# Optimization experiments

Measured on AMD Instinct MI355X. Metric: run time of the kernel, lower is better.

Reference implementation:

```python
import jax, jax.numpy as jnp
import numpy as np

OUTPUT_SIZE = 200
IOU_THRESHOLD = 0.5
SCORE_THRESHOLD = 0.01


def setup_inputs() -> dict:
    key = jax.random.key(0)
    k1, k2, k3 = jax.random.split(key, 3)
    B, N, C = 8, 2048, 80
    # well-formed boxes in [0,1]: (min_xy, max_xy)
    centers = jax.random.uniform(k1, (B, N, 2))
    sizes = jax.random.uniform(k2, (B, N, 2), minval=0.02, maxval=0.3)
    boxes = jnp.concatenate([centers - sizes / 2, centers + sizes / 2], axis=-1)
    scores = jax.random.uniform(k3, (B, N, C))
    x = jnp.concatenate([boxes, scores], axis=-1)  # [B, N, 4+C]
    return {"x": x}


def _box_iou(b):
    # b: [N, 4] (x1, y1, x2, y2) -> [N, N] IoU
    lt = jnp.maximum(b[:, None, :2], b[None, :, :2])
    rb = jnp.minimum(b[:, None, 2:], b[None, :, 2:])
    wh = jnp.maximum(rb - lt, 0.0)
    inter = wh[..., 0] * wh[..., 1]
    area = (b[:, 2] - b[:, 0]) * (b[:, 3] - b[:, 1])
    union = area[:, None] + area[None, :] - inter
    return inter / jnp.maximum(union, 1e-8)


def _nms_one_class(iou_b, scores_bc):
    # iou_b: [N, N] (shared across classes), scores_bc: [N]
    N = scores_bc.shape[0]
    order = jnp.argsort(-scores_bc)            # descending score order
    s_sorted = scores_bc[order]
    keep0 = s_sorted > SCORE_THRESHOLD
    pos = jnp.arange(N)

    def body(i, keep):
        row = iou_b[order[i]][order]           # IoU of i-th ranked box vs all, in sorted order
        sup = keep[i]                          # only a kept box suppresses others
        return keep & ~((row > IOU_THRESHOLD) & (pos > i) & sup)

    keep = jax.lax.fori_loop(0, N, body, keep0)
    # cap to max_output_size_per_class: keep only first OUTPUT_SIZE kept boxes
    rank = jnp.cumsum(keep.astype(jnp.int32))
    keep = keep & (rank <= OUTPUT_SIZE)
    sel_scores = jnp.where(keep, s_sorted, -jnp.inf)
    return sel_scores, order


def _combined_nms_one_batch(boxes_b, scores_b, iou_b):
    # boxes_b: [N,4], scores_b: [N,C], iou_b: [N,N]
    N, C = scores_b.shape
    sel_scores, order = jax.vmap(_nms_one_class, in_axes=(None, 1))(iou_b, scores_b)  # [C,N] each
    flat_scores = sel_scores.reshape(C * N)
    top_scores, top_idx = jax.lax.top_k(flat_scores, OUTPUT_SIZE)  # global top across classes
    cls = top_idx // N
    pos = top_idx % N
    box_idx = order[cls, pos]                  # original box indices
    top_boxes = jnp.clip(boxes_b[box_idx], 0.0, 1.0)  # clip_boxes=True
    valid = jnp.isfinite(top_scores)
    out = jnp.concatenate([
        cls.astype(jnp.float32)[:, None],
        top_scores[:, None],
        top_boxes,
    ], axis=-1)                                # [OUTPUT_SIZE, 6] = (cls, score, x1, y1, x2, y2)
    return jnp.where(valid[:, None], out, 0.0)


def reference(x):
    boxes = x[..., :4]                         # [B, N, 4]
    scores = x[..., 4:]                        # [B, N, C]
    iou = jax.vmap(_box_iou)(boxes)            # [B, N, N] (boxes shared across classes)
    return jax.vmap(_combined_nms_one_batch)(boxes, scores, iou)  # [B, OUTPUT_SIZE, 6]
```

## Files before the change

kernel.cpp:

```cpp
#include <hip/hip_runtime.h>
#include <stdint.h>

typedef unsigned long long u64;
typedef unsigned int u32;

#define NB 8
#define NN 2048
#define NC 80
#define ROW 84
#define OUT_K 200
#define IOU_T 0.5f
#define SCORE_T 0.01f
#define TGT 896
#define POOL 1024

__device__ __forceinline__ void ce_desc(u64* a, int i, int j, int k) {
    u64 a0 = a[i], a1 = a[i + j];
    bool up = ((i & k) == 0);
    if (up ? (a0 < a1) : (a0 > a1)) { a[i] = a1; a[i + j] = a0; }
}

__device__ __forceinline__ void ceg(u64& x, u64& y, bool up) {
    u64 a0 = x, a1 = y;
    if (up ? (a0 < a1) : (a0 > a1)) { x = a1; y = a0; }
}

__device__ __forceinline__ void wave_rounds512(u64* a, int base, int k, int jhi, int lane) {
    for (int j = jhi; j > 0; j >>= 1) {
        #pragma unroll
        for (int p = 0; p < 4; p++) {
            int r = lane + p * 64;
            int low = r & (j - 1);
            int high = (r & ~(j - 1)) << 1;
            ce_desc(a, base + (high | low), j, k);
        }
        __builtin_amdgcn_wave_barrier();
    }
}

__device__ __forceinline__ void wave_rounds256(u64* a, int base, int k, int jhi, int lane) {
    for (int j = jhi; j > 0; j >>= 1) {
        #pragma unroll
        for (int p = 0; p < 2; p++) {
            int r = lane + p * 64;
            int low = r & (j - 1);
            int high = (r & ~(j - 1)) << 1;
            ce_desc(a, base + (high | low), j, k);
        }
        __builtin_amdgcn_wave_barrier();
    }
}

__device__ __forceinline__ void pair_merge256(u64* a, int base, int off, int lane) {
    #pragma unroll
    for (int p0 = 0; p0 < 4; p0++) {
        int p = lane + p0 * 64;
        u64 xv = a[base + p];
        u64 yv = a[base + off + 255 - p];
        a[base + p] = xv > yv ? xv : yv;
    }
    __builtin_amdgcn_wave_barrier();
    wave_rounds256(a, base, 0x40000000, 128, lane);
}

__device__ __forceinline__ void sort2048(u64* key, int tid, int lane, int wv) {
    const int base = wv * 512;
    for (int k = 2; k <= 512; k <<= 1)
        wave_rounds512(key, base, k, k >> 1, lane);
    __syncthreads();
    #pragma unroll
    for (int p = 0; p < 4; p++) {
        int r = tid + p * 256;
        int low = r & 511, high = (r & ~511) << 1;
        ce_desc(key, high | low, 512, 1024);
    }
    __syncthreads();
    wave_rounds512(key, base, 1024, 256, lane);
    __syncthreads();
    #pragma unroll
    for (int p = 0; p < 4; p++) {
        int r = tid + p * 256;
        int low = r & 1023, high = (r & ~1023) << 1;
        ce_desc(key, high | low, 1024, 2048);
    }
    __syncthreads();
    #pragma unroll
    for (int p = 0; p < 4; p++) {
        int r = tid + p * 256;
        int low = r & 511, high = (r & ~511) << 1;
        ce_desc(key, high | low, 512, 2048);
    }
    __syncthreads();
    wave_rounds512(key, base, 2048, 256, lane);
    __syncthreads();
}

__device__ __forceinline__ void sort1024(u64* a, int tid, int lane, int wv) {
    const int t4 = tid * 4;
    const int sb = wv * 256;
    {
        u64 v0 = a[t4], v1 = a[t4 + 1], v2 = a[t4 + 2], v3 = a[t4 + 3];
        ceg(v0, v1, true);
        ceg(v2, v3, false);
        const bool d4 = ((t4 & 4) == 0);
        ceg(v0, v2, d4); ceg(v1, v3, d4);
        ceg(v0, v1, d4); ceg(v2, v3, d4);
        a[t4] = v0; a[t4 + 1] = v1; a[t4 + 2] = v2; a[t4 + 3] = v3;
    }
    __builtin_amdgcn_wave_barrier();
    for (int k = 8; k <= 256; k <<= 1) {
        for (int j = k >> 1; j >= 4; j >>= 1) {
            #pragma unroll
            for (int p = 0; p < 2; p++) {
                int r = lane + p * 64;
                int low = r & (j - 1);
                int high = (r & ~(j - 1)) << 1;
                ce_desc(a, sb + (high | low), j, k);
            }
            __builtin_amdgcn_wave_barrier();
        }
        {
            u64 v0 = a[t4], v1 = a[t4 + 1], v2 = a[t4 + 2], v3 = a[t4 + 3];
            const bool d = ((t4 & k) == 0);
            ceg(v0, v2, d); ceg(v1, v3, d);
            ceg(v0, v1, d); ceg(v2, v3, d);
            a[t4] = v0; a[t4 + 1] = v1; a[t4 + 2] = v2; a[t4 + 3] = v3;
        }
        __builtin_amdgcn_wave_barrier();
    }
    __syncthreads();
    #pragma unroll
    for (int p = 0; p < 2; p++) {
        int r = tid + p * 256;
        int low = r & 255, high = (r & ~255) << 1;
        ce_desc(a, high | low, 256, 512);
    }
    __syncthreads();
    for (int j = 128; j >= 4; j >>= 1) {
        #pragma unroll
        for (int p = 0; p < 2; p++) {
            int r = lane + p * 64;
            int low = r & (j - 1);
            int high = (r & ~(j - 1)) << 1;
            ce_desc(a, sb + (high | low), j, 512);
        }
        __builtin_amdgcn_wave_barrier();
    }
    {
        u64 v0 = a[t4], v1 = a[t4 + 1], v2 = a[t4 + 2], v3 = a[t4 + 3];
        const bool d = ((t4 & 512) == 0);
        ceg(v0, v2, d); ceg(v1, v3, d);
        ceg(v0, v1, d); ceg(v2, v3, d);
        a[t4] = v0; a[t4 + 1] = v1; a[t4 + 2] = v2; a[t4 + 3] = v3;
    }
    __syncthreads();
    #pragma unroll
    for (int p = 0; p < 2; p++) {
        int r = tid + p * 256;
        int low = r & 511, high = (r & ~511) << 1;
        ce_desc(a, high | low, 512, 1024);
    }
    __syncthreads();
    #pragma unroll
    for (int p = 0; p < 2; p++) {
        int r = tid + p * 256;
        int low = r & 255, high = (r & ~255) << 1;
        ce_desc(a, high | low, 256, 1024);
    }
    __syncthreads();
    for (int j = 128; j >= 4; j >>= 1) {
        #pragma unroll
        for (int p = 0; p < 2; p++) {
            int r = lane + p * 64;
            int low = r & (j - 1);
            int high = (r & ~(j - 1)) << 1;
            ce_desc(a, sb + (high | low), j, 1024);
        }
        __builtin_amdgcn_wave_barrier();
    }
    {
        u64 v0 = a[t4], v1 = a[t4 + 1], v2 = a[t4 + 2], v3 = a[t4 + 3];
        const bool d = ((t4 & 1024) == 0);
        ceg(v0, v2, d); ceg(v1, v3, d);
        ceg(v0, v1, d); ceg(v2, v3, d);
        a[t4] = v0; a[t4 + 1] = v1; a[t4 + 2] = v2; a[t4 + 3] = v3;
    }
    __syncthreads();
}

__device__ __forceinline__ bool iou_gt_half(float4 a, float aa, float4 b, float ab) {
    float ltx = fmaxf(a.x, b.x);
    float lty = fmaxf(a.y, b.y);
    float rbx = fminf(a.z, b.z);
    float rby = fminf(a.w, b.w);
    float wd = fmaxf(__fsub_rn(rbx, ltx), 0.0f);
    float hd = fmaxf(__fsub_rn(rby, lty), 0.0f);
    float inter = __fmul_rn(wd, hd);
    float uni = __fsub_rn(__fadd_rn(aa, ab), inter);
    float m = fmaxf(uni, 1e-8f);
    float d2 = __fmul_rn(2.0f, inter);
    bool sup = d2 > m;
    if (sup && (__fsub_rn(d2, m) <= __fmul_rn(m, 1.2e-7f)))
        sup = __fdiv_rn(inter, m) > IOU_T;
    return sup;
}

__device__ __forceinline__ void prefetch512(const u64* cand, const float* xb,
        float4* pbox, float* parea, int tid) {
    #pragma unroll
    for (int r = 0; r < 2; r++) {
        int i = r * 256 + tid;
        u64 k = cand[i];
        u32 orig = 2047u - (u32)(k & 0x7FFu);
        float4 bx = *(const float4*)(xb + (size_t)orig * ROW);
        pbox[i] = bx;
        parea[i] = __fmul_rn(__fsub_rn(bx.z, bx.x), __fsub_rn(bx.w, bx.y));
    }
    __syncthreads();
}

__device__ __forceinline__ int greedy(const u64* cand, int maxch, const float* xb,
        const float4* pbox, const float* parea,
        float4* s_cbox, float* s_car,
        float4* kept_box, float* kept_area, u64* kept_key,
        u64* s_sup, int* s_kept, int* s_done, int tid, int lane, int wv,
        int keptc_in) {
    if (tid == 0) { *s_kept = keptc_in; *s_done = 0; }
    __syncthreads();
    int keptc = keptc_in;
    for (int ch = 0; ch < maxch; ch++) {
        int n = ch * 64 + lane;
        u64 mykey = cand[n];
        float sc = __uint_as_float((u32)(mykey >> 32));
        bool valid = sc > SCORE_T;
        u64 vball = __ballot(valid);
        if (vball == 0ULL) break;

        float4 bx; float ar;
        const float4* cb; const float* ca;
        if (ch < 8) {
            bx = pbox[n];
            ar = parea[n];
            cb = pbox + ch * 64;
            ca = parea + ch * 64;
        } else {
            u32 orig = 2047u - (u32)(mykey & 0x7FFu);
            bx = *(const float4*)(xb + (size_t)orig * ROW);
            ar = __fmul_rn(__fsub_rn(bx.z, bx.x), __fsub_rn(bx.w, bx.y));
            if (wv == 0) { s_cbox[lane] = bx; s_car[lane] = ar; }
            __builtin_amdgcn_wave_barrier();
            cb = s_cbox; ca = s_car;
        }

        u64 colmask = 0ULL;
        if (wv == 0) {
            #pragma unroll 4
            for (int j = 0; j < 64; j++) {
                bool s = iou_gt_half(bx, ar, cb[j], ca[j]);
                colmask |= ((u64)s) << j;
            }
        } else {
            bool supA = false;
            int t = wv - 1;
            for (; t + 9 < keptc; t += 12) {
                float4 kb0 = kept_box[t],     kb1 = kept_box[t + 3];
                float4 kb2 = kept_box[t + 6], kb3 = kept_box[t + 9];
                float ka0 = kept_area[t],     ka1 = kept_area[t + 3];
                float ka2 = kept_area[t + 6], ka3 = kept_area[t + 9];
                bool s0 = iou_gt_half(bx, ar, kb0, ka0);
                bool s1 = iou_gt_half(bx, ar, kb1, ka1);
                bool s2 = iou_gt_half(bx, ar, kb2, ka2);
                bool s3 = iou_gt_half(bx, ar, kb3, ka3);
                supA = supA | ((s0 | s1) | (s2 | s3));
            }
            for (; t < keptc; t += 3)
                supA = supA | iou_gt_half(bx, ar, kept_box[t], kept_area[t]);
            u64 supm = __ballot(supA);
            if (lane == 0) s_sup[wv] = supm;
        }
        __syncthreads();

        if (wv == 0) {
            u64 alive = vball & ~s_sup[1] & ~s_sup[2] & ~s_sup[3];
            int kept = keptc;
            u64 keptbits = 0ULL;
            int donef = 0;
            while (alive) {
                int bsel = (int)__builtin_ctzll(alive);
                keptbits |= 1ULL << bsel;
                kept++;
                if (kept >= OUT_K) { donef = 1; break; }
                alive &= alive - 1;
                if (!alive) break;
                alive &= ~__ballot(((colmask >> bsel) & 1ULL) != 0ULL);
            }
            u32 rank = (u32)__popcll(keptbits & ((1ULL << lane) - 1ULL));
            if ((keptbits >> lane) & 1ULL) {
                int idx = keptc + (int)rank;
                kept_key[idx] = mykey;
                kept_box[idx] = bx;
                kept_area[idx] = ar;
            }
            if (lane == 0) { *s_kept = kept; if (donef) *s_done = 1; }
        }
        __syncthreads();
        keptc = *s_kept;
        if (*s_done) break;
        if (__popcll(vball) < 64) break;
    }
    __syncthreads();
    return keptc;
}

__global__ __launch_bounds__(256) void transpose_kernel(
        const float* __restrict__ x, float* __restrict__ st) {
    const int t = blockIdx.x;
    const int b = t >> 5;
    const int rb = t & 31;
    const int tid = threadIdx.x;
    __shared__ float lds[64 * 85];

    const float* src = x + ((size_t)b * NN + (size_t)rb * 64) * ROW;
    #pragma unroll
    for (int q = 0; q < 6; q++) {
        int i4 = q * 256 + tid;
        if (i4 < 1344) {
            float4 v = *(const float4*)(src + (size_t)i4 * 4);
            int r = i4 / 21;
            int kq = (i4 % 21) * 4;
            float* d = lds + r * 85 + kq;
            d[0] = v.x; d[1] = v.y; d[2] = v.z; d[3] = v.w;
        }
    }
    __syncthreads();
    const int n0 = rb * 64;
    #pragma unroll
    for (int q = 0; q < 20; q++) {
        int j = q * 256 + tid;
        int c = j >> 6;
        int r = j & 63;
        st[(size_t)(b * NC + c) * NN + n0 + r] = lds[r * 85 + 4 + c];
    }
}

__global__ __launch_bounds__(256) void nms_kernel(
        const float* __restrict__ x, const float* __restrict__ scores_t,
        u64* __restrict__ cand_key) {
    const int bc = blockIdx.x;
    const int b = bc / NC;
    const int c = bc % NC;
    const int tid = threadIdx.x;
    const int lane = tid & 63;
    const int wv = tid >> 6;

    __shared__ __align__(16) u64 arr[2048];
    u64* comp = arr;
    u32* hist = (u32*)(arr + 1024);
    __shared__ __align__(16) float4 s_pbox[512];
    __shared__ float s_parea[512];
    __shared__ __align__(16) float4 s_cbox[64];
    __shared__ float s_car[64];
    __shared__ float4 kept_box[OUT_K];
    __shared__ float kept_area[OUT_K];
    __shared__ u64 kept_key[OUT_K];
    __shared__ u64 s_sup[4];
    __shared__ u32 s_wsum[4];
    __shared__ u32 s_cnt, s_m;
    __shared__ int s_kept, s_done, s_thr;

    const float* xb = x + (size_t)b * NN * ROW;
    const float* sct = scores_t + (size_t)(b * NC + c) * NN;

    hist[tid] = 0;
    __syncthreads();
    float scv[8];
    #pragma unroll
    for (int w = 0; w < 8; w++) {
        int n = w * 256 + tid;
        float sc = sct[n];
        scv[w] = sc;
        int bin = (int)(sc * 256.0f); bin = bin > 255 ? 255 : bin;
        atomicAdd(&hist[bin], 1u);
    }
    __syncthreads();

    u32 cnt_mine = hist[tid];
    u32 incl = cnt_mine;
    #pragma unroll
    for (int off = 1; off < 64; off <<= 1) {
        u32 v = __shfl_down(incl, off, 64);
        if (lane + off < 64) incl += v;
    }
    if (lane == 0) s_wsum[wv] = incl;
    __syncthreads();
    u32 above = 0;
    #pragma unroll
    for (int w = 0; w < 4; w++) above += (w > wv) ? s_wsum[w] : 0;
    const u32 suf = incl + above;

    if (tid == 0) s_thr = 2;
    __syncthreads();
    if (suf >= TGT && suf - cnt_mine < TGT) s_thr = tid;
    __syncthreads();
    int t1 = s_thr;
    if (tid == t1) s_m = suf;
    __syncthreads();
    u32 m_tot = s_m;

    bool fb = (m_tot > POOL);
    int kept = 0;
    if (!fb) {
        if (tid == 0) s_cnt = 0;
        __syncthreads();
        #pragma unroll
        for (int w = 0; w < 8; w++) {
            float sc = scv[w];
            int bin = (int)(sc * 256.0f); bin = bin > 255 ? 255 : bin;
            if (bin >= t1) {
                int n = w * 256 + tid;
                u32 p = atomicAdd(&s_cnt, 1u);
                comp[p] = ((u64)__float_as_uint(sc) << 32) | (u64)(2047 - n);
            }
        }
        __syncthreads();
        for (int i = tid; i < POOL; i += 256) if (i >= (int)m_tot) comp[i] = 0ULL;
        __syncthreads();
        sort1024(comp, tid, lane, wv);
        prefetch512(comp, xb, s_pbox, s_parea, tid);
        kept = greedy(comp, POOL / 64, xb, s_pbox, s_parea, s_cbox, s_car,
                      kept_box, kept_area, kept_key,
                      s_sup, &s_kept, &s_done, tid, lane, wv, 0);

        while (kept < OUT_K && t1 > 2) {
            u32 T2 = m_tot + TGT;
            if (tid == 0) s_thr = 2;
            __syncthreads();
            if (suf >= T2 && suf - cnt_mine < T2) s_thr = tid;
            __syncthreads();
            int t2 = s_thr;
            if (tid == t2) s_m = suf;
            __syncthreads();
            u32 m2 = s_m;
            u32 size = m2 - m_tot;
            if (size == 0) break;
            if (size > POOL) { fb = true; break; }
            if (tid == 0) s_cnt = 0;
            __syncthreads();
            #pragma unroll
            for (int w = 0; w < 8; w++) {
                float sc = scv[w];
                int bin = (int)(sc * 256.0f); bin = bin > 255 ? 255 : bin;
                if (bin >= t2 && bin < t1) {
                    int n = w * 256 + tid;
                    u32 p = atomicAdd(&s_cnt, 1u);
                    comp[p] = ((u64)__float_as_uint(sc) << 32) | (u64)(2047 - n);
                }
            }
            __syncthreads();
            for (int i = tid; i < POOL; i += 256) if (i >= (int)size) comp[i] = 0ULL;
            __syncthreads();
            sort1024(comp, tid, lane, wv);
            prefetch512(comp, xb, s_pbox, s_parea, tid);
            kept = greedy(comp, POOL / 64, xb, s_pbox, s_parea, s_cbox, s_car,
                          kept_box, kept_area, kept_key,
                          s_sup, &s_kept, &s_done, tid, lane, wv, kept);
            m_tot = m2; t1 = t2;
        }
    }
    if (fb) {
        __syncthreads();
        #pragma unroll
        for (int w = 0; w < 8; w++) {
            int n = w * 256 + tid;
            arr[n] = ((u64)__float_as_uint(scv[w]) << 32) | (u64)(2047 - n);
        }
        __syncthreads();
        sort2048(arr, tid, lane, wv);
        prefetch512(arr, xb, s_pbox, s_parea, tid);
        kept = greedy(arr, 32, xb, s_pbox, s_parea, s_cbox, s_car,
                      kept_box, kept_area, kept_key,
                      s_sup, &s_kept, &s_done, tid, lane, wv, 0);
    }

    const int base_o = bc * OUT_K;
    if (tid < OUT_K) {
        u64 ok = 0ULL;
        if (tid < kept) {
            u64 kk = kept_key[tid];
            u32 flat = (u32)(c * OUT_K + tid);
            u32 orig = 2047u - (u32)(kk & 0x7FFu);
            ok = (kk & 0xFFFFFFFF00000000ULL) |
                 ((u64)(0x3FFFu - flat) << 11) | (u64)orig;
        }
        cand_key[base_o + tid] = ok;
    }
}

__global__ __launch_bounds__(256) void merge8_kernel(u64* __restrict__ cand_key) {
    const int blk = blockIdx.x;
    const int b = blk / 10;
    const int g = blk % 10;
    const int tid = threadIdx.x;
    const int lane = tid & 63;
    const int wv = tid >> 6;
    __shared__ __align__(16) u64 seg[2048];

    u64* src = cand_key + (size_t)(b * NC + g * 8) * OUT_K;

    #pragma unroll
    for (int q = 0; q < 8; q++) {
        seg[q * 256 + tid] = (tid < OUT_K) ? src[q * OUT_K + tid] : 0ULL;
    }
    __syncthreads();
    pair_merge256(seg, wv * 512, 256, lane);
    __syncthreads();
    if (wv < 2) pair_merge256(seg, wv * 1024, 512, lane);
    __syncthreads();
    if (wv == 0) pair_merge256(seg, 0, 1024, lane);
    __syncthreads();
    src[tid] = seg[tid];
}

__global__ __launch_bounds__(256) void final_kernel(
        const float* __restrict__ x, const u64* __restrict__ cand_key,
        float* __restrict__ out) {
    const int b = blockIdx.x;
    const int tid = threadIdx.x;
    const int lane = tid & 63;
    const int wv = tid >> 6;
    __shared__ __align__(16) u64 seg[2560];

    #pragma unroll
    for (int q = 0; q < 10; q++) {
        seg[q * 256 + tid] = cand_key[(size_t)(b * NC + q * 8) * OUT_K + tid];
    }
    __syncthreads();
    pair_merge256(seg, wv * 512, 256, lane);
    __syncthreads();
    if (wv == 0) pair_merge256(seg, 0, 512, lane);
    else if (wv == 1) pair_merge256(seg, 1024, 512, lane);
    else if (wv == 2) pair_merge256(seg, 2048, 256, lane);
    __syncthreads();
    if (wv == 0) pair_merge256(seg, 0, 1024, lane);
    __syncthreads();
    if (wv == 0) pair_merge256(seg, 0, 2048, lane);
    __syncthreads();

    const float* xb = x + (size_t)b * NN * ROW;
    if (tid < OUT_K) {
        u64 kk = seg[tid];
        float* o = out + ((size_t)b * OUT_K + tid) * 6;
        if (kk == 0ULL) {
            o[0] = 0.f; o[1] = 0.f; o[2] = 0.f; o[3] = 0.f; o[4] = 0.f; o[5] = 0.f;
        } else {
            u32 lo = (u32)(kk & 0xFFFFFFFFu);
            u32 flat = 0x3FFFu - ((lo >> 11) & 0x3FFFu);
            int cls = flat / OUT_K;
            u32 n = lo & 0x7FFu;
            float scf = __uint_as_float((u32)(kk >> 32));
            float4 bx = *(const float4*)(xb + (size_t)n * ROW);
            o[0] = (float)cls;
            o[1] = scf;
            o[2] = fminf(fmaxf(bx.x, 0.0f), 1.0f);
            o[3] = fminf(fmaxf(bx.y, 0.0f), 1.0f);
            o[4] = fminf(fmaxf(bx.z, 0.0f), 1.0f);
            o[5] = fminf(fmaxf(bx.w, 0.0f), 1.0f);
        }
    }
}

extern "C" void kernel_launch(void* const* d_in, const int* in_sizes, int n_in,
                              void* d_out, int out_size, void* d_ws, size_t ws_size,
                              hipStream_t stream) {
    const float* x = (const float*)d_in[0];
    float* out = (float*)d_out;
    u64* cand_key = (u64*)d_ws;
    float* scores_t = (float*)((char*)d_ws + 1024 * 1024);
    transpose_kernel<<<NB * 32, 256, 0, stream>>>(x, scores_t);
    nms_kernel<<<NB * NC, 256, 0, stream>>>(x, scores_t, cand_key);
    merge8_kernel<<<NB * 10, 256, 0, stream>>>(cand_key);
    final_kernel<<<NB, 256, 0, stream>>>(x, cand_key, out);
}
```

Before: 143.8 us.

## Double NMS block to 512 threads, split greedy work across eight waves

The per-class NMS kernel moves from 256 to 512 threads. The greedy column-mask IoU work is split between waves 0 and 4, and checks against already kept boxes are spread over six waves instead of three. Candidate compaction now uses wave-aggregated ballot plus a single atomic per wave instead of one atomic per element. The sorts keep their 4-wave structure, with the upper waves idle except in the cross-wave compare stages, which adds occupancy and barrier costs for the extra threads.

```diff
diff --git a/kernel.cpp b/kernel.cpp
--- a/kernel.cpp
+++ b/kernel.cpp
@@ -64,126 +64,135 @@
 }
 
 __device__ __forceinline__ void sort2048(u64* key, int tid, int lane, int wv) {
-    const int base = wv * 512;
-    for (int k = 2; k <= 512; k <<= 1)
-        wave_rounds512(key, base, k, k >> 1, lane);
-    __syncthreads();
-    #pragma unroll
-    for (int p = 0; p < 4; p++) {
-        int r = tid + p * 256;
+    if (wv < 4) {
+        const int base = wv * 512;
+        for (int k = 2; k <= 512; k <<= 1)
+            wave_rounds512(key, base, k, k >> 1, lane);
+    }
+    __syncthreads();
+    #pragma unroll
+    for (int p = 0; p < 2; p++) {
+        int r = tid + p * 512;
         int low = r & 511, high = (r & ~511) << 1;
         ce_desc(key, high | low, 512, 1024);
     }
     __syncthreads();
-    wave_rounds512(key, base, 1024, 256, lane);
-    __syncthreads();
-    #pragma unroll
-    for (int p = 0; p < 4; p++) {
-        int r = tid + p * 256;
+    if (wv < 4) wave_rounds512(key, wv * 512, 1024, 256, lane);
+    __syncthreads();
+    #pragma unroll
+    for (int p = 0; p < 2; p++) {
+        int r = tid + p * 512;
         int low = r & 1023, high = (r & ~1023) << 1;
         ce_desc(key, high | low, 1024, 2048);
     }
     __syncthreads();
     #pragma unroll
-    for (int p = 0; p < 4; p++) {
-        int r = tid + p * 256;
+    for (int p = 0; p < 2; p++) {
+        int r = tid + p * 512;
         int low = r & 511, high = (r & ~511) << 1;
         ce_desc(key, high | low, 512, 2048);
     }
     __syncthreads();
-    wave_rounds512(key, base, 2048, 256, lane);
+    if (wv < 4) wave_rounds512(key, wv * 512, 2048, 256, lane);
     __syncthreads();
 }
 
 __device__ __forceinline__ void sort1024(u64* a, int tid, int lane, int wv) {
-    const int t4 = tid * 4;
-    const int sb = wv * 256;
+    if (wv < 4) {
+        const int t4 = tid * 4;
+        const int sb = wv * 256;
+        {
+            u64 v0 = a[t4], v1 = a[t4 + 1], v2 = a[t4 + 2], v3 = a[t4 + 3];
+            ceg(v0, v1, true);
+            ceg(v2, v3, false);
+            const bool d4 = ((t4 & 4) == 0);
+            ceg(v0, v2, d4); ceg(v1, v3, d4);
+            ceg(v0, v1, d4); ceg(v2, v3, d4);
+            a[t4] = v0; a[t4 + 1] = v1; a[t4 + 2] = v2; a[t4 + 3] = v3;
+        }
+        __builtin_amdgcn_wave_barrier();
+        for (int k = 8; k <= 256; k <<= 1) {
+            for (int j = k >> 1; j >= 4; j >>= 1) {
+                #pragma unroll
+                for (int p = 0; p < 2; p++) {
+                    int r = lane + p * 64;
+                    int low = r & (j - 1);
+                    int high = (r & ~(j - 1)) << 1;
+                    ce_desc(a, sb + (high | low), j, k);
+                }
+                __builtin_amdgcn_wave_barrier();
+            }
+            {
+                u64 v0 = a[t4], v1 = a[t4 + 1], v2 = a[t4 + 2], v3 = a[t4 + 3];
+                const bool d = ((t4 & k) == 0);
+                ceg(v0, v2, d); ceg(v1, v3, d);
+                ceg(v0, v1, d); ceg(v2, v3, d);
+                a[t4] = v0; a[t4 + 1] = v1; a[t4 + 2] = v2; a[t4 + 3] = v3;
+            }
+            __builtin_amdgcn_wave_barrier();
+        }
+    }
+    __syncthreads();
     {
-        u64 v0 = a[t4], v1 = a[t4 + 1], v2 = a[t4 + 2], v3 = a[t4 + 3];
-        ceg(v0, v1, true);
-        ceg(v2, v3, false);
-        const bool d4 = ((t4 & 4) == 0);
-        ceg(v0, v2, d4); ceg(v1, v3, d4);
-        ceg(v0, v1, d4); ceg(v2, v3, d4);
-        a[t4] = v0; a[t4 + 1] = v1; a[t4 + 2] = v2; a[t4 + 3] = v3;
-    }
-    __builtin_amdgcn_wave_barrier();
-    for (int k = 8; k <= 256; k <<= 1) {
-        for (int j = k >> 1; j >= 4; j >>= 1) {
+        int r = tid;
+        int low = r & 255, high = (r & ~255) << 1;
+        ce_desc(a, high | low, 256, 512);
+    }
+    __syncthreads();
+    if (wv < 4) {
+        const int t4 = tid * 4;
+        const int sb = wv * 256;
+        for (int j = 128; j >= 4; j >>= 1) {
             #pragma unroll
             for (int p = 0; p < 2; p++) {
                 int r = lane + p * 64;
                 int low = r & (j - 1);
                 int high = (r & ~(j - 1)) << 1;
-                ce_desc(a, sb + (high | low), j, k);
+                ce_desc(a, sb + (high | low), j, 512);
             }
             __builtin_amdgcn_wave_barrier();
         }
         {
             u64 v0 = a[t4], v1 = a[t4 + 1], v2 = a[t4 + 2], v3 = a[t4 + 3];
-            const bool d = ((t4 & k) == 0);
+            const bool d = ((t4 & 512) == 0);
             ceg(v0, v2, d); ceg(v1, v3, d);
             ceg(v0, v1, d); ceg(v2, v3, d);
             a[t4] = v0; a[t4 + 1] = v1; a[t4 + 2] = v2; a[t4 + 3] = v3;
         }
-        __builtin_amdgcn_wave_barrier();
-    }
-    __syncthreads();
-    #pragma unroll
-    for (int p = 0; p < 2; p++) {
-        int r = tid + p * 256;
-        int low = r & 255, high = (r & ~255) << 1;
-        ce_desc(a, high | low, 256, 512);
-    }
-    __syncthreads();
-    for (int j = 128; j >= 4; j >>= 1) {
-        #pragma unroll
-        for (int p = 0; p < 2; p++) {
-            int r = lane + p * 64;
-            int low = r & (j - 1);
-            int high = (r & ~(j - 1)) << 1;
-            ce_desc(a, sb + (high | low), j, 512);
-        }
-        __builtin_amdgcn_wave_barrier();
-    }
+    }
+    __syncthreads();
     {
-        u64 v0 = a[t4], v1 = a[t4 + 1], v2 = a[t4 + 2], v3 = a[t4 + 3];
-        const bool d = ((t4 & 512) == 0);
-        ceg(v0, v2, d); ceg(v1, v3, d);
-        ceg(v0, v1, d); ceg(v2, v3, d);
-        a[t4] = v0; a[t4 + 1] = v1; a[t4 + 2] = v2; a[t4 + 3] = v3;
-    }
-    __syncthreads();
-    #pragma unroll
-    for (int p = 0; p < 2; p++) {
-        int r = tid + p * 256;
+        int r = tid;
         int low = r & 511, high = (r & ~511) << 1;
         ce_desc(a, high | low, 512, 1024);
     }
     __syncthreads();
-    #pragma unroll
-    for (int p = 0; p < 2; p++) {
-        int r = tid + p * 256;
+    {
+        int r = tid;
         int low = r & 255, high = (r & ~255) << 1;
         ce_desc(a, high | low, 256, 1024);
     }
     __syncthreads();
-    for (int j = 128; j >= 4; j >>= 1) {
-        #pragma unroll
-        for (int p = 0; p < 2; p++) {
-            int r = lane + p * 64;
-            int low = r & (j - 1);
-            int high = (r & ~(j - 1)) << 1;
-            ce_desc(a, sb + (high | low), j, 1024);
-        }
-        __builtin_amdgcn_wave_barrier();
-    }
-    {
-        u64 v0 = a[t4], v1 = a[t4 + 1], v2 = a[t4 + 2], v3 = a[t4 + 3];
-        const bool d = ((t4 & 1024) == 0);
-        ceg(v0, v2, d); ceg(v1, v3, d);
-        ceg(v0, v1, d); ceg(v2, v3, d);
-        a[t4] = v0; a[t4 + 1] = v1; a[t4 + 2] = v2; a[t4 + 3] = v3;
+    if (wv < 4) {
+        const int t4 = tid * 4;
+        const int sb = wv * 256;
+        for (int j = 128; j >= 4; j >>= 1) {
+            #pragma unroll
+            for (int p = 0; p < 2; p++) {
+                int r = lane + p * 64;
+                int low = r & (j - 1);
+                int high = (r & ~(j - 1)) << 1;
+                ce_desc(a, sb + (high | low), j, 1024);
+            }
+            __builtin_amdgcn_wave_barrier();
+        }
+        {
+            u64 v0 = a[t4], v1 = a[t4 + 1], v2 = a[t4 + 2], v3 = a[t4 + 3];
+            const bool d = ((t4 & 1024) == 0);
+            ceg(v0, v2, d); ceg(v1, v3, d);
+            ceg(v0, v1, d); ceg(v2, v3, d);
+            a[t4] = v0; a[t4 + 1] = v1; a[t4 + 2] = v2; a[t4 + 3] = v3;
+        }
     }
     __syncthreads();
 }
@@ -205,23 +214,35 @@
     return sup;
 }
 
+__device__ __forceinline__ float bcast(float v, int sl) {
+    return __int_as_float(__builtin_amdgcn_readlane(__float_as_int(v), sl));
+}
+
 __device__ __forceinline__ void prefetch512(const u64* cand, const float* xb,
         float4* pbox, float* parea, int tid) {
-    #pragma unroll
-    for (int r = 0; r < 2; r++) {
-        int i = r * 256 + tid;
-        u64 k = cand[i];
-        u32 orig = 2047u - (u32)(k & 0x7FFu);
-        float4 bx = *(const float4*)(xb + (size_t)orig * ROW);
-        pbox[i] = bx;
-        parea[i] = __fmul_rn(__fsub_rn(bx.z, bx.x), __fsub_rn(bx.w, bx.y));
-    }
-    __syncthreads();
+    u64 k = cand[tid];
+    u32 orig = 2047u - (u32)(k & 0x7FFu);
+    float4 bx = *(const float4*)(xb + (size_t)orig * ROW);
+    pbox[tid] = bx;
+    parea[tid] = __fmul_rn(__fsub_rn(bx.z, bx.x), __fsub_rn(bx.w, bx.y));
+    __syncthreads();
+}
+
+__device__ __forceinline__ void push_sel(u64* comp, u32* s_cnt, bool pred,
+                                         u64 key, int lane) {
+    u64 bal = __ballot(pred);
+    u32 base = 0;
+    if (lane == 0 && bal) base = atomicAdd(s_cnt, (u32)__popcll(bal));
+    base = (u32)__shfl((int)base, 0, 64);
+    if (pred) {
+        u32 off = (u32)__popcll(bal & ((1ULL << lane) - 1ULL));
+        comp[base + off] = key;
+    }
 }
 
 __device__ __forceinline__ int greedy(const u64* cand, int maxch, const float* xb,
         const float4* pbox, const float* parea,
-        float4* s_cbox, float* s_car,
+        float4* s_cbox, float* s_car, u64* s_cmhi,
         float4* kept_box, float* kept_area, u64* kept_key,
         u64* s_sup, int* s_kept, int* s_done, int tid, int lane, int wv,
         int keptc_in) {
@@ -247,33 +268,38 @@
             u32 orig = 2047u - (u32)(mykey & 0x7FFu);
             bx = *(const float4*)(xb + (size_t)orig * ROW);
             ar = __fmul_rn(__fsub_rn(bx.z, bx.x), __fsub_rn(bx.w, bx.y));
-            if (wv == 0) { s_cbox[lane] = bx; s_car[lane] = ar; }
+            if (wv == 0 || wv == 4) { s_cbox[lane] = bx; s_car[lane] = ar; }
             __builtin_amdgcn_wave_barrier();
             cb = s_cbox; ca = s_car;
         }
 
-        u64 colmask = 0ULL;
-        if (wv == 0) {
+        u64 cm_lo = 0ULL;
+        if (wv == 0 || wv == 4) {
+            u64 colmask = 0ULL;
+            const int j0 = (wv == 0) ? 0 : 32;
             #pragma unroll 4
-            for (int j = 0; j < 64; j++) {
+            for (int jj = 0; jj < 32; jj++) {
+                int j = j0 + jj;
                 bool s = iou_gt_half(bx, ar, cb[j], ca[j]);
                 colmask |= ((u64)s) << j;
             }
+            if (wv == 4) s_cmhi[lane] = colmask; else cm_lo = colmask;
         } else {
+            int widx = (wv < 4) ? (wv - 1) : (wv - 2);
             bool supA = false;
-            int t = wv - 1;
-            for (; t + 9 < keptc; t += 12) {
-                float4 kb0 = kept_box[t],     kb1 = kept_box[t + 3];
-                float4 kb2 = kept_box[t + 6], kb3 = kept_box[t + 9];
-                float ka0 = kept_area[t],     ka1 = kept_area[t + 3];
-                float ka2 = kept_area[t + 6], ka3 = kept_area[t + 9];
+            int t = widx;
+            for (; t + 18 < keptc; t += 24) {
+                float4 kb0 = kept_box[t],      kb1 = kept_box[t + 6];
+                float4 kb2 = kept_box[t + 12], kb3 = kept_box[t + 18];
+                float ka0 = kept_area[t],      ka1 = kept_area[t + 6];
+                float ka2 = kept_area[t + 12], ka3 = kept_area[t + 18];
                 bool s0 = iou_gt_half(bx, ar, kb0, ka0);
                 bool s1 = iou_gt_half(bx, ar, kb1, ka1);
                 bool s2 = iou_gt_half(bx, ar, kb2, ka2);
                 bool s3 = iou_gt_half(bx, ar, kb3, ka3);
                 supA = supA | ((s0 | s1) | (s2 | s3));
             }
-            for (; t < keptc; t += 3)
+            for (; t < keptc; t += 6)
                 supA = supA | iou_gt_half(bx, ar, kept_box[t], kept_area[t]);
             u64 supm = __ballot(supA);
             if (lane == 0) s_sup[wv] = supm;
@@ -281,7 +307,9 @@
         __syncthreads();
 
         if (wv == 0) {
-            u64 alive = vball & ~s_sup[1] & ~s_sup[2] & ~s_sup[3];
+            u64 colmask = cm_lo | s_cmhi[lane];
+            u64 alive = vball & ~s_sup[1] & ~s_sup[2] & ~s_sup[3]
+                              & ~s_sup[5] & ~s_sup[6] & ~s_sup[7];
             int kept = keptc;
             u64 keptbits = 0ULL;
             int donef = 0;
@@ -343,7 +371,7 @@
     }
 }
 
-__global__ __launch_bounds__(256) void nms_kernel(
+__global__ __launch_bounds__(512) void nms_kernel(
         const float* __restrict__ x, const float* __restrict__ scores_t,
         u64* __restrict__ cand_key) {
     const int bc = blockIdx.x;
@@ -360,10 +388,11 @@
     __shared__ float s_parea[512];
     __shared__ __align__(16) float4 s_cbox[64];
     __shared__ float s_car[64];
+    __shared__ u64 s_cmhi[64];
     __shared__ float4 kept_box[OUT_K];
     __shared__ float kept_area[OUT_K];
     __shared__ u64 kept_key[OUT_K];
-    __shared__ u64 s_sup[4];
+    __shared__ u64 s_sup[8];
     __shared__ u32 s_wsum[4];
     __shared__ u32 s_cnt, s_m;
     __shared__ int s_kept, s_done, s_thr;
@@ -371,12 +400,12 @@
     const float* xb = x + (size_t)b * NN * ROW;
     const float* sct = scores_t + (size_t)(b * NC + c) * NN;
 
-    hist[tid] = 0;
-    __syncthreads();
-    float scv[8];
-    #pragma unroll
-    for (int w = 0; w < 8; w++) {
-        int n = w * 256 + tid;
+    if (tid < 256) hist[tid] = 0;
+    __syncthreads();
+    float scv[4];
+    #pragma unroll
+    for (int w = 0; w < 4; w++) {
+        int n = w * 512 + tid;
         float sc = sct[n];
         scv[w] = sc;
         int bin = (int)(sc * 256.0f); bin = bin > 255 ? 255 : bin;
@@ -384,23 +413,28 @@
     }
     __syncthreads();
 
-    u32 cnt_mine = hist[tid];
-    u32 incl = cnt_mine;
-    #pragma unroll
-    for (int off = 1; off < 64; off <<= 1) {
-        u32 v = __shfl_down(incl, off, 64);
-        if (lane + off < 64) incl += v;
-    }
-    if (lane == 0) s_wsum[wv] = incl;
-    __syncthreads();
-    u32 above = 0;
-    #pragma unroll
-    for (int w = 0; w < 4; w++) above += (w > wv) ? s_wsum[w] : 0;
-    const u32 suf = incl + above;
+    u32 cnt_mine = 0, incl = 0, suf = 0;
+    if (tid < 256) {
+        cnt_mine = hist[tid];
+        incl = cnt_mine;
+        #pragma unroll
+        for (int off = 1; off < 64; off <<= 1) {
+            u32 v = __shfl_down(incl, off, 64);
+            if (lane + off < 64) incl += v;
+        }
+        if (lane == 0) s_wsum[wv] = incl;
+    }
+    __syncthreads();
+    if (tid < 256) {
+        u32 above = 0;
+        #pragma unroll
+        for (int w = 0; w < 4; w++) above += (w > wv) ? s_wsum[w] : 0;
+        suf = incl + above;
+    }
 
     if (tid == 0) s_thr = 2;
     __syncthreads();
-    if (suf >= TGT && suf - cnt_mine < TGT) s_thr = tid;
+    if (tid < 256 && suf >= TGT && suf - cnt_mine < TGT) s_thr = tid;
     __syncthreads();
     int t1 = s_thr;
     if (tid == t1) s_m = suf;
@@ -413,21 +447,19 @@
         if (tid == 0) s_cnt = 0;
         __syncthreads();
         #pragma unroll
-        for (int w = 0; w < 8; w++) {
+        for (int w = 0; w < 4; w++) {
             float sc = scv[w];
             int bin = (int)(sc * 256.0f); bin = bin > 255 ? 255 : bin;
-            if (bin >= t1) {
-                int n = w * 256 + tid;
-                u32 p = atomicAdd(&s_cnt, 1u);
-                comp[p] = ((u64)__float_as_uint(sc) << 32) | (u64)(2047 - n);
-            }
+            int n = w * 512 + tid;
+            u64 key = ((u64)__float_as_uint(sc) << 32) | (u64)(2047 - n);
+            push_sel(comp, &s_cnt, bin >= t1, key, lane);
         }
         __syncthreads();
-        for (int i = tid; i < POOL; i += 256) if (i >= (int)m_tot) comp[i] = 0ULL;
+        for (int i = tid; i < POOL; i += 512) if (i >= (int)m_tot) comp[i] = 0ULL;
         __syncthreads();
         sort1024(comp, tid, lane, wv);
         prefetch512(comp, xb, s_pbox, s_parea, tid);
-        kept = greedy(comp, POOL / 64, xb, s_pbox, s_parea, s_cbox, s_car,
+        kept = greedy(comp, POOL / 64, xb, s_pbox, s_parea, s_cbox, s_car, s_cmhi,
                       kept_box, kept_area, kept_key,
                       s_sup, &s_kept, &s_done, tid, lane, wv, 0);
 
@@ -435,7 +467,7 @@
             u32 T2 = m_tot + TGT;
             if (tid == 0) s_thr = 2;
             __syncthreads();
-            if (suf >= T2 && suf - cnt_mine < T2) s_thr = tid;
+            if (tid < 256 && suf >= T2 && suf - cnt_mine < T2) s_thr = tid;
             __syncthreads();
             int t2 = s_thr;
             if (tid == t2) s_m = suf;
@@ -447,21 +479,19 @@
             if (tid == 0) s_cnt = 0;
             __syncthreads();
             #pragma unroll
-            for (int w = 0; w < 8; w++) {
+            for (int w = 0; w < 4; w++) {
                 float sc = scv[w];
                 int bin = (int)(sc * 256.0f); bin = bin > 255 ? 255 : bin;
-                if (bin >= t2 && bin < t1) {
-                    int n = w * 256 + tid;
-                    u32 p = atomicAdd(&s_cnt, 1u);
-                    comp[p] = ((u64)__float_as_uint(sc) << 32) | (u64)(2047 - n);
-                }
+                int n = w * 512 + tid;
+                u64 key = ((u64)__float_as_uint(sc) << 32) | (u64)(2047 - n);
+                push_sel(comp, &s_cnt, bin >= t2 && bin < t1, key, lane);
             }
             __syncthreads();
-            for (int i = tid; i < POOL; i += 256) if (i >= (int)size) comp[i] = 0ULL;
+            for (int i = tid; i < POOL; i += 512) if (i >= (int)size) comp[i] = 0ULL;
             __syncthreads();
             sort1024(comp, tid, lane, wv);
             prefetch512(comp, xb, s_pbox, s_parea, tid);
-            kept = greedy(comp, POOL / 64, xb, s_pbox, s_parea, s_cbox, s_car,
+            kept = greedy(comp, POOL / 64, xb, s_pbox, s_parea, s_cbox, s_car, s_cmhi,
                           kept_box, kept_area, kept_key,
                           s_sup, &s_kept, &s_done, tid, lane, wv, kept);
             m_tot = m2; t1 = t2;
@@ -470,14 +500,14 @@
     if (fb) {
         __syncthreads();
         #pragma unroll
-        for (int w = 0; w < 8; w++) {
-            int n = w * 256 + tid;
+        for (int w = 0; w < 4; w++) {
+            int n = w * 512 + tid;
             arr[n] = ((u64)__float_as_uint(scv[w]) << 32) | (u64)(2047 - n);
         }
         __syncthreads();
         sort2048(arr, tid, lane, wv);
         prefetch512(arr, xb, s_pbox, s_parea, tid);
-        kept = greedy(arr, 32, xb, s_pbox, s_parea, s_cbox, s_car,
+        kept = greedy(arr, 32, xb, s_pbox, s_parea, s_cbox, s_car, s_cmhi,
                       kept_box, kept_area, kept_key,
                       s_sup, &s_kept, &s_done, tid, lane, wv, 0);
     }
@@ -577,7 +607,7 @@
     u64* cand_key = (u64*)d_ws;
     float* scores_t = (float*)((char*)d_ws + 1024 * 1024);
     transpose_kernel<<<NB * 32, 256, 0, stream>>>(x, scores_t);
-    nms_kernel<<<NB * NC, 256, 0, stream>>>(x, scores_t, cand_key);
+    nms_kernel<<<NB * NC, 512, 0, stream>>>(x, scores_t, cand_key);
     merge8_kernel<<<NB * 10, 256, 0, stream>>>(cand_key);
     final_kernel<<<NB, 256, 0, stream>>>(x, cand_key, out);
 }
```

Measured after the change: 238.8 us. 66.1% more time.

## Split intra-chunk IoU mask across all waves and prefetch 1024 candidate boxes

Applied to the files above, without the earlier changes.

The 64x64 intra-chunk IoU column-mask computation, previously done by wave 0 alone, is now split across all four waves, each handling 16 columns. Partial masks are combined through shared memory, and all four waves now check candidates against the kept-box list. The candidate box prefetch into shared memory grows from 512 to 1024 entries, so the first 16 chunks read boxes from LDS instead of global memory. In exchange, LDS use rises, which may lower occupancy, and the fallback path now uses a full block barrier instead of a wave barrier.

```diff
diff --git a/kernel.cpp b/kernel.cpp
--- a/kernel.cpp
+++ b/kernel.cpp
@@ -205,10 +205,10 @@
     return sup;
 }
 
-__device__ __forceinline__ void prefetch512(const u64* cand, const float* xb,
+__device__ __forceinline__ void prefetch1024(const u64* cand, const float* xb,
         float4* pbox, float* parea, int tid) {
     #pragma unroll
-    for (int r = 0; r < 2; r++) {
+    for (int r = 0; r < 4; r++) {
         int i = r * 256 + tid;
         u64 k = cand[i];
         u32 orig = 2047u - (u32)(k & 0x7FFu);
@@ -221,7 +221,7 @@
 
 __device__ __forceinline__ int greedy(const u64* cand, int maxch, const float* xb,
         const float4* pbox, const float* parea,
-        float4* s_cbox, float* s_car,
+        float4* s_cbox, float* s_car, u64* s_cm,
         float4* kept_box, float* kept_area, u64* kept_key,
         u64* s_sup, int* s_kept, int* s_done, int tid, int lane, int wv,
         int keptc_in) {
@@ -238,7 +238,7 @@
 
         float4 bx; float ar;
         const float4* cb; const float* ca;
-        if (ch < 8) {
+        if (ch < 16) {
             bx = pbox[n];
             ar = parea[n];
             cb = pbox + ch * 64;
@@ -248,32 +248,36 @@
             bx = *(const float4*)(xb + (size_t)orig * ROW);
             ar = __fmul_rn(__fsub_rn(bx.z, bx.x), __fsub_rn(bx.w, bx.y));
             if (wv == 0) { s_cbox[lane] = bx; s_car[lane] = ar; }
-            __builtin_amdgcn_wave_barrier();
+            __syncthreads();
             cb = s_cbox; ca = s_car;
         }
 
-        u64 colmask = 0ULL;
-        if (wv == 0) {
+        u64 cm = 0ULL;
+        {
+            const int j0 = wv * 16;
             #pragma unroll 4
-            for (int j = 0; j < 64; j++) {
+            for (int jj = 0; jj < 16; jj++) {
+                int j = j0 + jj;
                 bool s = iou_gt_half(bx, ar, cb[j], ca[j]);
-                colmask |= ((u64)s) << j;
-            }
-        } else {
+                cm |= ((u64)s) << j;
+            }
+            s_cm[wv * 64 + lane] = cm;
+        }
+        {
             bool supA = false;
-            int t = wv - 1;
-            for (; t + 9 < keptc; t += 12) {
-                float4 kb0 = kept_box[t],     kb1 = kept_box[t + 3];
-                float4 kb2 = kept_box[t + 6], kb3 = kept_box[t + 9];
-                float ka0 = kept_area[t],     ka1 = kept_area[t + 3];
-                float ka2 = kept_area[t + 6], ka3 = kept_area[t + 9];
+            int t = wv;
+            for (; t + 12 < keptc; t += 16) {
+                float4 kb0 = kept_box[t],     kb1 = kept_box[t + 4];
+                float4 kb2 = kept_box[t + 8], kb3 = kept_box[t + 12];
+                float ka0 = kept_area[t],     ka1 = kept_area[t + 4];
+                float ka2 = kept_area[t + 8], ka3 = kept_area[t + 12];
                 bool s0 = iou_gt_half(bx, ar, kb0, ka0);
                 bool s1 = iou_gt_half(bx, ar, kb1, ka1);
                 bool s2 = iou_gt_half(bx, ar, kb2, ka2);
                 bool s3 = iou_gt_half(bx, ar, kb3, ka3);
                 supA = supA | ((s0 | s1) | (s2 | s3));
             }
-            for (; t < keptc; t += 3)
+            for (; t < keptc; t += 4)
                 supA = supA | iou_gt_half(bx, ar, kept_box[t], kept_area[t]);
             u64 supm = __ballot(supA);
             if (lane == 0) s_sup[wv] = supm;
@@ -281,7 +285,8 @@
         __syncthreads();
 
         if (wv == 0) {
-            u64 alive = vball & ~s_sup[1] & ~s_sup[2] & ~s_sup[3];
+            u64 colmask = cm | s_cm[64 + lane] | s_cm[128 + lane] | s_cm[192 + lane];
+            u64 alive = vball & ~s_sup[0] & ~s_sup[1] & ~s_sup[2] & ~s_sup[3];
             int kept = keptc;
             u64 keptbits = 0ULL;
             int donef = 0;
@@ -356,10 +361,11 @@
     __shared__ __align__(16) u64 arr[2048];
     u64* comp = arr;
     u32* hist = (u32*)(arr + 1024);
-    __shared__ __align__(16) float4 s_pbox[512];
-    __shared__ float s_parea[512];
+    __shared__ __align__(16) float4 s_pbox[1024];
+    __shared__ float s_parea[1024];
     __shared__ __align__(16) float4 s_cbox[64];
     __shared__ float s_car[64];
+    __shared__ u64 s_cm[256];
     __shared__ float4 kept_box[OUT_K];
     __shared__ float kept_area[OUT_K];
     __shared__ u64 kept_key[OUT_K];
@@ -426,8 +432,8 @@
         for (int i = tid; i < POOL; i += 256) if (i >= (int)m_tot) comp[i] = 0ULL;
         __syncthreads();
         sort1024(comp, tid, lane, wv);
-        prefetch512(comp, xb, s_pbox, s_parea, tid);
-        kept = greedy(comp, POOL / 64, xb, s_pbox, s_parea, s_cbox, s_car,
+        prefetch1024(comp, xb, s_pbox, s_parea, tid);
+        kept = greedy(comp, POOL / 64, xb, s_pbox, s_parea, s_cbox, s_car, s_cm,
                       kept_box, kept_area, kept_key,
                       s_sup, &s_kept, &s_done, tid, lane, wv, 0);
 
@@ -460,8 +466,8 @@
             for (int i = tid; i < POOL; i += 256) if (i >= (int)size) comp[i] = 0ULL;
             __syncthreads();
             sort1024(comp, tid, lane, wv);
-            prefetch512(comp, xb, s_pbox, s_parea, tid);
-            kept = greedy(comp, POOL / 64, xb, s_pbox, s_parea, s_cbox, s_car,
+            prefetch1024(comp, xb, s_pbox, s_parea, tid);
+            kept = greedy(comp, POOL / 64, xb, s_pbox, s_parea, s_cbox, s_car, s_cm,
                           kept_box, kept_area, kept_key,
                           s_sup, &s_kept, &s_done, tid, lane, wv, kept);
             m_tot = m2; t1 = t2;
@@ -476,8 +482,8 @@
         }
         __syncthreads();
         sort2048(arr, tid, lane, wv);
-        prefetch512(arr, xb, s_pbox, s_parea, tid);
-        kept = greedy(arr, 32, xb, s_pbox, s_parea, s_cbox, s_car,
+        prefetch1024(arr, xb, s_pbox, s_parea, tid);
+        kept = greedy(arr, 32, xb, s_pbox, s_parea, s_cbox, s_car, s_cm,
                       kept_box, kept_area, kept_key,
                       s_sup, &s_kept, &s_done, tid, lane, wv, 0);
     }
```

After: 133.1 us. -7.5%, faster.
